# Performance work log

Measured on AMD Instinct MI355X. Metric: run time of the kernel, lower is better.

The kernel has to match this reference:

```python
import jax, jax.numpy as jnp
import numpy as np

EPS = 1e-3


def batchnorm(x, gamma, beta):
    # BatchNorm1d in training mode: batch mean and biased variance over dim 0
    mean = jnp.mean(x, axis=0)
    var = jnp.var(x, axis=0)  # biased, matches torch BN normalization
    return (x - mean) * jax.lax.rsqrt(var + EPS) * gamma + beta


def setup_inputs() -> dict:
    key = jax.random.key(0)
    ks = jax.random.split(key, 12)
    N, C_in, C_out, G = 400000, 64, 128, 30000
    points_xyz = jax.random.normal(ks[0], (N, 3), dtype=jnp.float32) * 10.0
    feat_all = jax.random.normal(ks[1], (N, C_in), dtype=jnp.float32)
    unq_inv = jax.random.randint(ks[2], (N,), 0, G, dtype=jnp.int32)
    s_in = 1.0 / np.sqrt(C_in)
    s3 = 1.0 / np.sqrt(3.0)
    return {
        "points_xyz": points_xyz,
        "feat_all": feat_all,
        "unq_inv": unq_inv,
        "W_pre": jax.random.uniform(ks[3], (C_in, C_out), jnp.float32, -s_in, s_in),
        "b_pre": jax.random.uniform(ks[4], (C_out,), jnp.float32, -s_in, s_in),
        "g1": jnp.ones((C_out,), jnp.float32),
        "be1": jnp.zeros((C_out,), jnp.float32),
        "Wp1": jax.random.uniform(ks[5], (3, C_out), jnp.float32, -s3, s3),
        "bp1": jax.random.uniform(ks[6], (C_out,), jnp.float32, -s3, s3),
        "Wp2": jax.random.uniform(ks[7], (3, C_out), jnp.float32, -s3, s3),
        "bp2": jax.random.uniform(ks[8], (C_out,), jnp.float32, -s3, s3),
        "g2": jnp.ones((C_out,), jnp.float32),
        "be2": jnp.zeros((C_out,), jnp.float32),
        "num_segments": 30000,
    }


def reference(points_xyz, feat_all, unq_inv, W_pre, b_pre, g1, be1,
              Wp1, bp1, Wp2, bp2, g2, be2, num_segments):
    p = jnp.floor(points_xyz)                       # [N, 3]
    feat = batchnorm(feat_all @ W_pre + b_pre, g1, be1)  # [N, C_out]
    pw1 = p @ Wp1 + bp1                             # [N, C_out]
    pw2 = p @ Wp2 + bp2                             # [N, C_out]
    feat_weight = pw1 * feat                        # [N, C_out]
    feat_add = jax.ops.segment_sum(feat_weight, unq_inv,
                                   num_segments=num_segments)  # [G, C_out]
    feat_add = feat_add[unq_inv]                    # gather back: [N, C_out]
    out = pw2 * feat - feat_add
    out = jax.nn.relu(batchnorm(out, g2, be2))
    return out
```

## Files before the change

kernel.cpp:

```cpp
#include <hip/hip_runtime.h>
#include <hip/hip_bf16.h>

typedef unsigned int u32;
typedef unsigned short u16;
typedef __attribute__((ext_vector_type(8))) short short8;
typedef __attribute__((ext_vector_type(4))) float floatx4;

#define COUT 128
#define GSEG 30000
#define BN_EPS 1e-3f

__device__ __forceinline__ u32 f2bf(float x) {
    u32 u = __float_as_uint(x);
    return (u + 0x7fffu + ((u >> 16) & 1u)) >> 16;
}
__device__ __forceinline__ float bf2f(u32 b) { return __uint_as_float(b << 16); }

__device__ __forceinline__ void unpack8(uint4 v, float* f) {
    f[0] = __uint_as_float(v.x << 16); f[1] = __uint_as_float(v.x & 0xffff0000u);
    f[2] = __uint_as_float(v.y << 16); f[3] = __uint_as_float(v.y & 0xffff0000u);
    f[4] = __uint_as_float(v.z << 16); f[5] = __uint_as_float(v.z & 0xffff0000u);
    f[6] = __uint_as_float(v.w << 16); f[7] = __uint_as_float(v.w & 0xffff0000u);
}

__global__ __launch_bounds__(512) void k_prep_w(
    const float* __restrict__ W, u16* __restrict__ wt_f)
{
    int t = threadIdx.x;
    for (int f = t; f < 8192; f += 512) {
        int ch = f >> 3, e = f & 7;
        int ct = ch >> 7, ks = (ch >> 6) & 1, lane = ch & 63;
        int c = ct * 16 + (lane & 15);
        int k = ks * 32 + (lane >> 4) * 8 + e;
        float w = W[k * 128 + c];
        u32 hb = f2bf(w);
        float lo = w - bf2f(hb);
        wt_f[f] = (u16)hb;
        wt_f[8192 + f] = (u16)f2bf(lo);
    }
}

__global__ __launch_bounds__(512) void k_gemm_bn1(
    const float* __restrict__ A, const u16* __restrict__ wt_f,
    const float* __restrict__ bias, const int* __restrict__ unq, int* __restrict__ cnt,
    u16* __restrict__ lin, float* __restrict__ sum1, float* __restrict__ sumsq1, int n)
{
    __shared__ union {
        u16 w[16384];
        u16 pack[128 * 136];
    } sm;
    __shared__ float sSum[128], sSq[128];

    const int t = threadIdx.x;
    const int row0 = blockIdx.x * 128;
    if (t < 128) { sSum[t] = 0.f; sSq[t] = 0.f; }

    if (t < 128 && row0 + t < n) atomicAdd(&cnt[unq[row0 + t]], 1);

    const int lane = t & 63, wv = t >> 6;
    const int r = lane & 15, q = lane >> 4;
    const int rw0 = wv * 16;
    const int row_a = row0 + rw0 + r;
    const bool ok = row_a < n;

    const float* ap = A + (size_t)row_a * 64;
    float4 av[4];
#pragma unroll
    for (int ks = 0; ks < 2; ks++) {
        av[ks * 2]     = ok ? *(const float4*)(ap + ks * 32 + q * 8)     : make_float4(0.f, 0.f, 0.f, 0.f);
        av[ks * 2 + 1] = ok ? *(const float4*)(ap + ks * 32 + q * 8 + 4) : make_float4(0.f, 0.f, 0.f, 0.f);
    }

#pragma unroll
    for (int j = 0; j < 4; j++) {
        int chunk = j * 512 + t;
        uint4 v = *(const uint4*)(wt_f + chunk * 8);
        *(uint4*)&sm.w[chunk * 8] = v;
    }

    short8 arh[2], arl[2];
#pragma unroll
    for (int ks = 0; ks < 2; ks++) {
        float vv[8] = {av[ks * 2].x, av[ks * 2].y, av[ks * 2].z, av[ks * 2].w,
                       av[ks * 2 + 1].x, av[ks * 2 + 1].y, av[ks * 2 + 1].z, av[ks * 2 + 1].w};
#pragma unroll
        for (int i = 0; i < 8; i++) {
            u32 hb = f2bf(vv[i]);
            float lo = vv[i] - bf2f(hb);
            arh[ks][i] = (short)(u16)hb;
            arl[ks][i] = (short)(u16)f2bf(lo);
        }
    }

    floatx4 acc[8];
#pragma unroll
    for (int ct = 0; ct < 8; ct++) acc[ct] = (floatx4){0.f, 0.f, 0.f, 0.f};

    __syncthreads();

    const int fbase = lane * 8;
#pragma unroll
    for (int ct = 0; ct < 8; ct++) {
#pragma unroll
        for (int ks = 0; ks < 2; ks++) {
            int fo = (ct * 2 + ks) * 512 + fbase;
            short8 wh = *(const short8*)&sm.w[fo];
            short8 wl = *(const short8*)&sm.w[8192 + fo];
            acc[ct] = __builtin_amdgcn_mfma_f32_16x16x32_bf16(arh[ks], wh, acc[ct], 0, 0, 0);
            acc[ct] = __builtin_amdgcn_mfma_f32_16x16x32_bf16(arl[ks], wh, acc[ct], 0, 0, 0);
            acc[ct] = __builtin_amdgcn_mfma_f32_16x16x32_bf16(arh[ks], wl, acc[ct], 0, 0, 0);
        }
    }
    __syncthreads();

#pragma unroll
    for (int ct = 0; ct < 8; ct++) {
        int c = ct * 16 + r;
        float bv = bias[c];
        float ssum = 0.f, ssq = 0.f;
#pragma unroll
        for (int i = 0; i < 4; i++) {
            int lrow = rw0 + q * 4 + i;
            float v = acc[ct][i] + bv;
            if (row0 + lrow >= n) v = 0.f;
            ssum += v; ssq += v * v;
            sm.pack[lrow * 136 + c] = (u16)f2bf(v);
        }
        ssum += __shfl_xor(ssum, 16, 64); ssq += __shfl_xor(ssq, 16, 64);
        ssum += __shfl_xor(ssum, 32, 64); ssq += __shfl_xor(ssq, 32, 64);
        if (lane < 16) { atomicAdd(&sSum[c], ssum); atomicAdd(&sSq[c], ssq); }
    }
    __syncthreads();

#pragma unroll
    for (int j = 0; j < 4; j++) {
        int f = t + j * 512;
        int row = f >> 4, c0 = (f & 15) << 3;
        if (row0 + row < n) {
            uint4 v = *(const uint4*)&sm.pack[row * 136 + c0];
            *(uint4*)(lin + (size_t)(row0 + row) * 128 + c0) = v;
        }
    }
    if (t < 128) { atomicAdd(&sum1[t], sSum[t]); atomicAdd(&sumsq1[t], sSq[t]); }
}

__global__ void k_fin(const float* __restrict__ sum, const float* __restrict__ sumsq,
                      const float* __restrict__ g, const float* __restrict__ be,
                      float* __restrict__ scale, float* __restrict__ shift, float inv_n)
{
    int c = threadIdx.x;
    float mean = sum[c] * inv_n;
    float var = sumsq[c] * inv_n - mean * mean;
    float sc = g[c] * rsqrtf(var + BN_EPS);
    scale[c] = sc;
    shift[c] = be[c] - mean * sc;
}

__global__ __launch_bounds__(1024) void k_scan(const int* __restrict__ cnt,
                                               int* __restrict__ offs,
                                               int* __restrict__ cursor)
{
    __shared__ int wsum[16];
    int t = threadIdx.x, lane = t & 63, wv = t >> 6;
    int base = t * 32;
    int v[32];
    int s = 0;
    if (base + 32 <= GSEG) {
        const int4* cp = (const int4*)(cnt + base);
#pragma unroll
        for (int j = 0; j < 8; j++) {
            int4 q = cp[j];
            v[j * 4 + 0] = q.x; v[j * 4 + 1] = q.y; v[j * 4 + 2] = q.z; v[j * 4 + 3] = q.w;
            s += q.x + q.y + q.z + q.w;
        }
    } else {
#pragma unroll
        for (int j = 0; j < 32; j++) {
            int idx = base + j;
            int x = (idx < GSEG) ? cnt[idx] : 0;
            v[j] = x; s += x;
        }
    }
    int x = s;
#pragma unroll
    for (int d = 1; d < 64; d <<= 1) {
        int u = __shfl_up(x, d, 64);
        if (lane >= d) x += u;
    }
    if (lane == 63) wsum[wv] = x;
    __syncthreads();
    if (t < 16) {
        int w = wsum[t];
#pragma unroll
        for (int d = 1; d < 16; d <<= 1) {
            int u = __shfl_up(w, d, 16);
            if (t >= d) w += u;
        }
        wsum[t] = w;
    }
    __syncthreads();
    int run = (wv ? wsum[wv - 1] : 0) + (x - s);
#pragma unroll
    for (int j = 0; j < 32; j++) {
        int idx = base + j;
        if (idx < GSEG) { offs[idx] = run; cursor[idx] = run; }
        run += v[j];
    }
    if (t == 1023) offs[GSEG] = wsum[15];
}

__global__ __launch_bounds__(256) void k_scatter_idx(const int* __restrict__ unq,
                                                     int* __restrict__ cursor,
                                                     int* __restrict__ order, int n)
{
    int i = blockIdx.x * 256 + threadIdx.x;
    if (i < n) {
        int pos = atomicAdd(&cursor[unq[i]], 1);
        order[pos] = i;
    }
}

__global__ __launch_bounds__(256) void k_segsum(
    const u16* __restrict__ lin, const float* __restrict__ xyz,
    const int* __restrict__ order, const int* __restrict__ offs,
    const float* __restrict__ scale1, const float* __restrict__ shift1,
    const float* __restrict__ Wp1, const float* __restrict__ bp1,
    const float* __restrict__ Wp2, const float* __restrict__ bp2,
    float* __restrict__ feat_add, float* __restrict__ sum2, float* __restrict__ sumsq2,
    int nseg)
{
    __shared__ float sSum[128], sSq[128];
    const int t = threadIdx.x;
    if (t < 128) { sSum[t] = 0.f; sSq[t] = 0.f; }
    __syncthreads();
    const int wave = t >> 6, lane = t & 63;
    const int c = lane * 2;
    const float wa0x = Wp1[c],     wa0y = Wp1[128 + c],     wa0z = Wp1[256 + c],     ba0 = bp1[c];
    const float wa1x = Wp1[c + 1], wa1y = Wp1[128 + c + 1], wa1z = Wp1[256 + c + 1], ba1 = bp1[c + 1];
    const float wb0x = Wp2[c],     wb0y = Wp2[128 + c],     wb0z = Wp2[256 + c],     bb0 = bp2[c];
    const float wb1x = Wp2[c + 1], wb1y = Wp2[128 + c + 1], wb1z = Wp2[256 + c + 1], bb1 = bp2[c + 1];
    const float sc0 = scale1[c], sh0 = shift1[c];
    const float sc1 = scale1[c + 1], sh1 = shift1[c + 1];
    float rs0 = 0.f, rs1 = 0.f, rq0 = 0.f, rq1 = 0.f;
    const int stride = gridDim.x * 4;
    for (int s = blockIdx.x * 4 + wave; s < nseg; s += stride) {
        const int beg = offs[s], end = offs[s + 1];
        const int m = end - beg;
        int rowv = 0; float fxv = 0.f, fyv = 0.f, fzv = 0.f;
        if (lane < m) {
            rowv = order[beg + lane];
            fxv = floorf(xyz[rowv * 3]);
            fyv = floorf(xyz[rowv * 3 + 1]);
            fzv = floorf(xyz[rowv * 3 + 2]);
        }
        float acc0 = 0.f, acc1 = 0.f, p10 = 0.f, p11 = 0.f, p20 = 0.f, p21 = 0.f;
        const int mm = m < 64 ? m : 64;
        for (int j = 0; j < mm; j++) {
            int row = __shfl(rowv, j, 64);
            float px = __shfl(fxv, j, 64);
            float py = __shfl(fyv, j, 64);
            float pz = __shfl(fzv, j, 64);
            u32 l2 = *(const u32*)(lin + (size_t)row * 128 + c);
            float fe0 = fmaf(__uint_as_float(l2 << 16), sc0, sh0);
            float fe1 = fmaf(__uint_as_float(l2 & 0xffff0000u), sc1, sh1);
            float pa0 = fmaf(px, wa0x, fmaf(py, wa0y, fmaf(pz, wa0z, ba0)));
            float pa1 = fmaf(px, wa1x, fmaf(py, wa1y, fmaf(pz, wa1z, ba1)));
            float pb0 = fmaf(px, wb0x, fmaf(py, wb0y, fmaf(pz, wb0z, bb0)));
            float pb1 = fmaf(px, wb1x, fmaf(py, wb1y, fmaf(pz, wb1z, bb1)));
            acc0 = fmaf(pa0, fe0, acc0);
            acc1 = fmaf(pa1, fe1, acc1);
            float t0 = pb0 * fe0, t1 = pb1 * fe1;
            p10 += t0; p11 += t1;
            p20 = fmaf(t0, t0, p20); p21 = fmaf(t1, t1, p21);
        }
        for (int j = 64; j < m; j++) {
            int row = order[beg + j];
            float px = floorf(xyz[row * 3]);
            float py = floorf(xyz[row * 3 + 1]);
            float pz = floorf(xyz[row * 3 + 2]);
            u32 l2 = *(const u32*)(lin + (size_t)row * 128 + c);
            float fe0 = fmaf(__uint_as_float(l2 << 16), sc0, sh0);
            float fe1 = fmaf(__uint_as_float(l2 & 0xffff0000u), sc1, sh1);
            float pa0 = fmaf(px, wa0x, fmaf(py, wa0y, fmaf(pz, wa0z, ba0)));
            float pa1 = fmaf(px, wa1x, fmaf(py, wa1y, fmaf(pz, wa1z, ba1)));
            float pb0 = fmaf(px, wb0x, fmaf(py, wb0y, fmaf(pz, wb0z, bb0)));
            float pb1 = fmaf(px, wb1x, fmaf(py, wb1y, fmaf(pz, wb1z, bb1)));
            acc0 = fmaf(pa0, fe0, acc0);
            acc1 = fmaf(pa1, fe1, acc1);
            float t0 = pb0 * fe0, t1 = pb1 * fe1;
            p10 += t0; p11 += t1;
            p20 = fmaf(t0, t0, p20); p21 = fmaf(t1, t1, p21);
        }
        float2 st; st.x = acc0; st.y = acc1;
        *(float2*)(feat_add + (size_t)s * 128 + c) = st;
        float fm = (float)m;
        rs0 += p10 - fm * acc0;
        rs1 += p11 - fm * acc1;
        rq0 += fmaf(fm * acc0, acc0, p20 - 2.f * acc0 * p10);
        rq1 += fmaf(fm * acc1, acc1, p21 - 2.f * acc1 * p11);
    }
    atomicAdd(&sSum[c], rs0); atomicAdd(&sSum[c + 1], rs1);
    atomicAdd(&sSq[c], rq0);  atomicAdd(&sSq[c + 1], rq1);
    __syncthreads();
    if (t < 128) { atomicAdd(&sum2[t], sSum[t]); atomicAdd(&sumsq2[t], sSq[t]); }
}

__global__ __launch_bounds__(256) void k_final(
    const u16* __restrict__ lin, const float* __restrict__ xyz, const int* __restrict__ unq,
    const float* __restrict__ scale1, const float* __restrict__ shift1,
    const float* __restrict__ Wp2, const float* __restrict__ bp2,
    const float* __restrict__ feat_add,
    const float* __restrict__ scale2, const float* __restrict__ shift2,
    float* __restrict__ out, int n)
{
    __shared__ float sS[128], sH[128], sW3[384], sB[128], sS2[128], sH2[128];
    int t = threadIdx.x;
    if (t < 128) {
        sS[t] = scale1[t]; sH[t] = shift1[t]; sB[t] = bp2[t];
        sW3[t] = Wp2[t]; sW3[128 + t] = Wp2[128 + t]; sW3[256 + t] = Wp2[256 + t];
        sS2[t] = scale2[t]; sH2[t] = shift2[t];
    }
    __syncthreads();
    int row = blockIdx.x * 16 + (t >> 4);
    if (row >= n) return;
    int c0 = (t & 15) * 8;
    uint4 l8 = *(const uint4*)(lin + (size_t)row * 128 + c0);
    float f[8];
    unpack8(l8, f);
    float px = floorf(xyz[row * 3 + 0]);
    float py = floorf(xyz[row * 3 + 1]);
    float pz = floorf(xyz[row * 3 + 2]);
    int g = unq[row];
    const float4* fa = (const float4*)(feat_add + (size_t)g * 128 + c0);
    float4 fa0 = fa[0], fa1 = fa[1];
    float fav[8] = {fa0.x, fa0.y, fa0.z, fa0.w, fa1.x, fa1.y, fa1.z, fa1.w};
    float o[8];
#pragma unroll
    for (int j = 0; j < 8; j++) {
        int c = c0 + j;
        float fe = fmaf(f[j], sS[c], sH[c]);
        float pw = fmaf(px, sW3[c], fmaf(py, sW3[128 + c], fmaf(pz, sW3[256 + c], sB[c])));
        float v = pw * fe - fav[j];
        v = fmaf(v, sS2[c], sH2[c]);
        o[j] = v > 0.f ? v : 0.f;
    }
    float4 s0, s1;
    s0.x = o[0]; s0.y = o[1]; s0.z = o[2]; s0.w = o[3];
    s1.x = o[4]; s1.y = o[5]; s1.z = o[6]; s1.w = o[7];
    float* op = out + (size_t)row * 128 + c0;
    *(float4*)op = s0;
    *(float4*)(op + 4) = s1;
}

extern "C" void kernel_launch(void* const* d_in, const int* in_sizes, int n_in,
                              void* d_out, int out_size, void* d_ws, size_t ws_size,
                              hipStream_t stream)
{
    const float* xyz      = (const float*)d_in[0];
    const float* feat_all = (const float*)d_in[1];
    const int*   unq      = (const int*)d_in[2];
    const float* W_pre    = (const float*)d_in[3];
    const float* b_pre    = (const float*)d_in[4];
    const float* g1       = (const float*)d_in[5];
    const float* be1      = (const float*)d_in[6];
    const float* Wp1      = (const float*)d_in[7];
    const float* bp1      = (const float*)d_in[8];
    const float* Wp2      = (const float*)d_in[9];
    const float* bp2      = (const float*)d_in[10];
    const float* g2       = (const float*)d_in[11];
    const float* be2      = (const float*)d_in[12];
    (void)n_in; (void)out_size; (void)ws_size;

    const int n = in_sizes[0] / 3;

    char* ws = (char*)d_ws;
    float* stats  = (float*)ws;
    float* sum1   = stats;       float* sumsq1 = stats + 128;
    float* sum2   = stats + 256; float* sumsq2 = stats + 384;
    float* scale1 = stats + 512; float* shift1 = stats + 640;
    float* scale2 = stats + 768; float* shift2 = stats + 896;
    int*   cnt      = (int*)(ws + 4096);
    int*   offs     = (int*)(ws + 124160);
    int*   cursor   = (int*)(ws + 244224);
    int*   order    = (int*)(ws + 364288);
    u16*   wt_f     = (u16*)(ws + 1964544 - 32768);
    float* feat_add = (float*)(ws + 1964544);
    u16*   lin      = (u16*)(ws + 17324544);

    hipMemsetAsync(d_ws, 0, 124160, stream);

    k_prep_w<<<1, 512, 0, stream>>>(W_pre, wt_f);
    k_gemm_bn1<<<(n + 127) / 128, 512, 0, stream>>>(feat_all, wt_f, b_pre, unq, cnt,
                                                    lin, sum1, sumsq1, n);
    k_fin<<<1, 128, 0, stream>>>(sum1, sumsq1, g1, be1, scale1, shift1, 1.0f / n);

    k_scan<<<1, 1024, 0, stream>>>(cnt, offs, cursor);
    k_scatter_idx<<<(n + 255) / 256, 256, 0, stream>>>(unq, cursor, order, n);
    k_segsum<<<1876, 256, 0, stream>>>(lin, xyz, order, offs, scale1, shift1,
                                       Wp1, bp1, Wp2, bp2, feat_add, sum2, sumsq2, GSEG);
    k_fin<<<1, 128, 0, stream>>>(sum2, sumsq2, g2, be2, scale2, shift2, 1.0f / n);
    k_final<<<(n + 15) / 16, 256, 0, stream>>>(lin, xyz, unq, scale1, shift1, Wp2, bp2,
                                               feat_add, scale2, shift2, (float*)d_out, n);
}
```

Baseline: 553.1 us.

## Replicate BN stat accumulators across 32 slots and unroll segment-sum loop

The global per-channel sum and sum-of-squares atomics in the GEMM and segment-sum kernels now go to 32 replicated slots chosen by block index. The finalize kernel reduces those slots, which is meant to cut contention from thousands of blocks hitting the same 256 addresses. The segment-sum inner loop is also unrolled by two to expose more independent gathers. Its xyz read now uses a float2 load, which is only 4-byte aligned for odd rows. The workspace is reshuffled so buffers with disjoint lifetimes share memory (wt_f with cursor, cnt with order), and the memsets are resized to match.

```diff
diff --git a/kernel.cpp b/kernel.cpp
--- a/kernel.cpp
+++ b/kernel.cpp
@@ -9,6 +9,7 @@
 #define COUT 128
 #define GSEG 30000
 #define BN_EPS 1e-3f
+#define REP 32
 
 __device__ __forceinline__ u32 f2bf(float x) {
     u32 u = __float_as_uint(x);
@@ -43,7 +44,7 @@
 __global__ __launch_bounds__(512) void k_gemm_bn1(
     const float* __restrict__ A, const u16* __restrict__ wt_f,
     const float* __restrict__ bias, const int* __restrict__ unq, int* __restrict__ cnt,
-    u16* __restrict__ lin, float* __restrict__ sum1, float* __restrict__ sumsq1, int n)
+    u16* __restrict__ lin, float* __restrict__ sum1rep, float* __restrict__ sumsq1rep, int n)
 {
     __shared__ union {
         u16 w[16384];
@@ -141,16 +142,23 @@
             *(uint4*)(lin + (size_t)(row0 + row) * 128 + c0) = v;
         }
     }
-    if (t < 128) { atomicAdd(&sum1[t], sSum[t]); atomicAdd(&sumsq1[t], sSq[t]); }
-}
-
-__global__ void k_fin(const float* __restrict__ sum, const float* __restrict__ sumsq,
+    if (t < 128) {
+        int rep = (blockIdx.x & (REP - 1)) * 128;
+        atomicAdd(&sum1rep[rep + t], sSum[t]);
+        atomicAdd(&sumsq1rep[rep + t], sSq[t]);
+    }
+}
+
+__global__ void k_fin(const float* __restrict__ sumrep, const float* __restrict__ sqrep,
                       const float* __restrict__ g, const float* __restrict__ be,
                       float* __restrict__ scale, float* __restrict__ shift, float inv_n)
 {
     int c = threadIdx.x;
-    float mean = sum[c] * inv_n;
-    float var = sumsq[c] * inv_n - mean * mean;
+    float s = 0.f, q = 0.f;
+#pragma unroll
+    for (int r = 0; r < REP; r++) { s += sumrep[r * 128 + c]; q += sqrep[r * 128 + c]; }
+    float mean = s * inv_n;
+    float var = q * inv_n - mean * mean;
     float sc = g[c] * rsqrtf(var + BN_EPS);
     scale[c] = sc;
     shift[c] = be[c] - mean * sc;
@@ -226,7 +234,7 @@
     const float* __restrict__ scale1, const float* __restrict__ shift1,
     const float* __restrict__ Wp1, const float* __restrict__ bp1,
     const float* __restrict__ Wp2, const float* __restrict__ bp2,
-    float* __restrict__ feat_add, float* __restrict__ sum2, float* __restrict__ sumsq2,
+    float* __restrict__ feat_add, float* __restrict__ sum2rep, float* __restrict__ sumsq2rep,
     int nseg)
 {
     __shared__ float sSum[128], sSq[128];
@@ -249,13 +257,43 @@
         int rowv = 0; float fxv = 0.f, fyv = 0.f, fzv = 0.f;
         if (lane < m) {
             rowv = order[beg + lane];
-            fxv = floorf(xyz[rowv * 3]);
-            fyv = floorf(xyz[rowv * 3 + 1]);
+            float2 xy = *(const float2*)(xyz + rowv * 3);
+            fxv = floorf(xy.x);
+            fyv = floorf(xy.y);
             fzv = floorf(xyz[rowv * 3 + 2]);
         }
         float acc0 = 0.f, acc1 = 0.f, p10 = 0.f, p11 = 0.f, p20 = 0.f, p21 = 0.f;
         const int mm = m < 64 ? m : 64;
-        for (int j = 0; j < mm; j++) {
+        int j = 0;
+        for (; j + 2 <= mm; j += 2) {
+            int rowA = __shfl(rowv, j, 64),     rowB = __shfl(rowv, j + 1, 64);
+            float pxA = __shfl(fxv, j, 64),     pxB = __shfl(fxv, j + 1, 64);
+            float pyA = __shfl(fyv, j, 64),     pyB = __shfl(fyv, j + 1, 64);
+            float pzA = __shfl(fzv, j, 64),     pzB = __shfl(fzv, j + 1, 64);
+            u32 lA = *(const u32*)(lin + (size_t)rowA * 128 + c);
+            u32 lB = *(const u32*)(lin + (size_t)rowB * 128 + c);
+            float feA0 = fmaf(__uint_as_float(lA << 16), sc0, sh0);
+            float feA1 = fmaf(__uint_as_float(lA & 0xffff0000u), sc1, sh1);
+            float feB0 = fmaf(__uint_as_float(lB << 16), sc0, sh0);
+            float feB1 = fmaf(__uint_as_float(lB & 0xffff0000u), sc1, sh1);
+            float paA0 = fmaf(pxA, wa0x, fmaf(pyA, wa0y, fmaf(pzA, wa0z, ba0)));
+            float paA1 = fmaf(pxA, wa1x, fmaf(pyA, wa1y, fmaf(pzA, wa1z, ba1)));
+            float pbA0 = fmaf(pxA, wb0x, fmaf(pyA, wb0y, fmaf(pzA, wb0z, bb0)));
+            float pbA1 = fmaf(pxA, wb1x, fmaf(pyA, wb1y, fmaf(pzA, wb1z, bb1)));
+            float paB0 = fmaf(pxB, wa0x, fmaf(pyB, wa0y, fmaf(pzB, wa0z, ba0)));
+            float paB1 = fmaf(pxB, wa1x, fmaf(pyB, wa1y, fmaf(pzB, wa1z, ba1)));
+            float pbB0 = fmaf(pxB, wb0x, fmaf(pyB, wb0y, fmaf(pzB, wb0z, bb0)));
+            float pbB1 = fmaf(pxB, wb1x, fmaf(pyB, wb1y, fmaf(pzB, wb1z, bb1)));
+            acc0 = fmaf(paA0, feA0, acc0); acc1 = fmaf(paA1, feA1, acc1);
+            float tA0 = pbA0 * feA0, tA1 = pbA1 * feA1;
+            p10 += tA0; p11 += tA1;
+            p20 = fmaf(tA0, tA0, p20); p21 = fmaf(tA1, tA1, p21);
+            acc0 = fmaf(paB0, feB0, acc0); acc1 = fmaf(paB1, feB1, acc1);
+            float tB0 = pbB0 * feB0, tB1 = pbB1 * feB1;
+            p10 += tB0; p11 += tB1;
+            p20 = fmaf(tB0, tB0, p20); p21 = fmaf(tB1, tB1, p21);
+        }
+        for (; j < mm; j++) {
             int row = __shfl(rowv, j, 64);
             float px = __shfl(fxv, j, 64);
             float py = __shfl(fyv, j, 64);
@@ -273,8 +311,8 @@
             p10 += t0; p11 += t1;
             p20 = fmaf(t0, t0, p20); p21 = fmaf(t1, t1, p21);
         }
-        for (int j = 64; j < m; j++) {
-            int row = order[beg + j];
+        for (int jj = 64; jj < m; jj++) {
+            int row = order[beg + jj];
             float px = floorf(xyz[row * 3]);
             float py = floorf(xyz[row * 3 + 1]);
             float pz = floorf(xyz[row * 3 + 2]);
@@ -302,7 +340,11 @@
     atomicAdd(&sSum[c], rs0); atomicAdd(&sSum[c + 1], rs1);
     atomicAdd(&sSq[c], rq0);  atomicAdd(&sSq[c + 1], rq1);
     __syncthreads();
-    if (t < 128) { atomicAdd(&sum2[t], sSum[t]); atomicAdd(&sumsq2[t], sSq[t]); }
+    if (t < 128) {
+        int rep = (blockIdx.x & (REP - 1)) * 128;
+        atomicAdd(&sum2rep[rep + t], sSum[t]);
+        atomicAdd(&sumsq2rep[rep + t], sSq[t]);
+    }
 }
 
 __global__ __launch_bounds__(256) void k_final(
@@ -374,31 +416,35 @@
     const int n = in_sizes[0] / 3;
 
     char* ws = (char*)d_ws;
-    float* stats  = (float*)ws;
-    float* sum1   = stats;       float* sumsq1 = stats + 128;
-    float* sum2   = stats + 256; float* sumsq2 = stats + 384;
-    float* scale1 = stats + 512; float* shift1 = stats + 640;
-    float* scale2 = stats + 768; float* shift2 = stats + 896;
-    int*   cnt      = (int*)(ws + 4096);
-    int*   offs     = (int*)(ws + 124160);
-    int*   cursor   = (int*)(ws + 244224);
-    int*   order    = (int*)(ws + 364288);
-    u16*   wt_f     = (u16*)(ws + 1964544 - 32768);
-    float* feat_add = (float*)(ws + 1964544);
-    u16*   lin      = (u16*)(ws + 17324544);
-
-    hipMemsetAsync(d_ws, 0, 124160, stream);
+    float* sum1rep   = (float*)(ws + 0);
+    float* sumsq1rep = (float*)(ws + 16384);
+    float* sum2rep   = (float*)(ws + 32768);
+    float* sumsq2rep = (float*)(ws + 49152);
+    float* scale1    = (float*)(ws + 65536);
+    float* shift1    = (float*)(ws + 66048);
+    float* scale2    = (float*)(ws + 66560);
+    float* shift2    = (float*)(ws + 67072);
+    int*   offs      = (int*)(ws + 67584);
+    int*   cursor    = (int*)(ws + 187648);
+    u16*   wt_f      = (u16*)(ws + 187648);
+    int*   order     = (int*)(ws + 307648);
+    int*   cnt       = (int*)(ws + 307648);
+    float* feat_add  = (float*)(ws + 1907648);
+    u16*   lin       = (u16*)(ws + 17267648);
+
+    hipMemsetAsync(ws, 0, 65536, stream);
+    hipMemsetAsync(ws + 307648, 0, 120000, stream);
 
     k_prep_w<<<1, 512, 0, stream>>>(W_pre, wt_f);
     k_gemm_bn1<<<(n + 127) / 128, 512, 0, stream>>>(feat_all, wt_f, b_pre, unq, cnt,
-                                                    lin, sum1, sumsq1, n);
-    k_fin<<<1, 128, 0, stream>>>(sum1, sumsq1, g1, be1, scale1, shift1, 1.0f / n);
+                                                    lin, sum1rep, sumsq1rep, n);
+    k_fin<<<1, 128, 0, stream>>>(sum1rep, sumsq1rep, g1, be1, scale1, shift1, 1.0f / n);
 
     k_scan<<<1, 1024, 0, stream>>>(cnt, offs, cursor);
     k_scatter_idx<<<(n + 255) / 256, 256, 0, stream>>>(unq, cursor, order, n);
     k_segsum<<<1876, 256, 0, stream>>>(lin, xyz, order, offs, scale1, shift1,
-                                       Wp1, bp1, Wp2, bp2, feat_add, sum2, sumsq2, GSEG);
-    k_fin<<<1, 128, 0, stream>>>(sum2, sumsq2, g2, be2, scale2, shift2, 1.0f / n);
+                                       Wp1, bp1, Wp2, bp2, feat_add, sum2rep, sumsq2rep, GSEG);
+    k_fin<<<1, 128, 0, stream>>>(sum2rep, sumsq2rep, g2, be2, scale2, shift2, 1.0f / n);
     k_final<<<(n + 15) / 16, 256, 0, stream>>>(lin, xyz, unq, scale1, shift1, Wp2, bp2,
                                                feat_add, scale2, shift2, (float*)d_out, n);
 }
```

New measurement: 529.8 us. 1.04x faster.
